# Kernel tuning notes

Measured on AMD Instinct MI355X. Metric: run time of the kernel, lower is better.

## Reference

```python
import jax, jax.numpy as jnp
import numpy as np

B_, L_, H_ = 2, 2048, 2048          # batch, seq_len, hidden_size
I_, N_, NH, P_ = 4096, 128, 64, 64   # intermediate, ssm_state, num_heads, head_dim
K_, CH = 4, 256                      # conv kernel, chunk size
DT_MIN, DT_MAX = 0.0, 1e10


def setup_inputs() -> dict:
    key = jax.random.key(0)
    ks = jax.random.split(key, 8)
    conv_dim = I_ + 2 * N_
    proj_out = 2 * (I_ + N_) + NH
    return {
        "hidden_states": jax.random.normal(ks[0], (B_, L_, H_), jnp.float32),
        "W_in": jax.random.normal(ks[1], (proj_out, H_), jnp.float32) * 0.02,
        "conv_w": jax.random.normal(ks[2], (conv_dim, 1, K_), jnp.float32) * 0.2,
        "conv_b": jnp.zeros((conv_dim,), jnp.float32),
        "dt_bias": jax.random.uniform(ks[3], (NH,), jnp.float32),
        "A_log": jnp.log(jax.random.uniform(ks[4], (NH,), jnp.float32, 1.0, 16.0)),
        "D": jnp.ones((NH,), jnp.float32),
        "norm_w": jnp.ones((I_,), jnp.float32),
        "W_out": jax.random.normal(ks[5], (H_, I_), jnp.float32) * 0.02,
    }


def _segsum(x):
    # stable segment-sum: out[..., i, j] = sum_{k=j+1..i} x[..., k] for i>=j, else -inf
    T = x.shape[-1]
    xr = jnp.broadcast_to(x[..., None], x.shape + (T,))
    lower = jnp.tril(jnp.ones((T, T), bool), -1)
    s = jnp.cumsum(jnp.where(lower, xr, 0.0), axis=-2)
    return jnp.where(jnp.tril(jnp.ones((T, T), bool)), s, -jnp.inf)


def reference(hidden_states, W_in, conv_w, conv_b, dt_bias, A_log, D, norm_w, W_out):
    b, L, _ = hidden_states.shape
    proj = hidden_states @ W_in.T                       # (b, L, 2*(I+N)+H)
    z, xBC, dt = jnp.split(proj, [I_, 2 * I_ + 2 * N_], axis=-1)

    # depthwise causal conv1d + silu
    x_t = xBC.transpose(0, 2, 1)                        # (b, conv_dim, L)
    conv = jax.lax.conv_general_dilated(
        x_t, conv_w, (1,), [(K_ - 1, 0)],
        dimension_numbers=("NCH", "OIH", "NCH"), feature_group_count=I_ + 2 * N_)
    xBC = jax.nn.silu((conv + conv_b[None, :, None]).transpose(0, 2, 1))
    x, Bm, Cm = jnp.split(xBC, [I_, I_ + N_], axis=-1)  # (b,L,I) (b,L,N) (b,L,N)

    # ---- SSD naive (chunked state-space-duality scan) ----
    A = -jnp.exp(A_log.astype(jnp.float32))             # (h,)
    dt = jnp.clip(jax.nn.softplus(dt + dt_bias), DT_MIN, DT_MAX)  # (b,L,h)
    x4 = x.reshape(b, L, NH, P_)
    pad = (-L) % CH
    padf = lambda t: jnp.pad(t, [(0, 0), (0, pad)] + [(0, 0)] * (t.ndim - 2))
    D_res = D[None, None, :, None] * padf(x4)           # (b, Lp, h, p)
    xs = padf(x4 * dt[..., None])
    Ah = padf(A[None, None, :] * dt)                    # (b, Lp, h)
    Bc, Cc = padf(Bm), padf(Cm)
    c = (L + pad) // CH
    xs = xs.reshape(b, c, CH, NH, P_)                   # (b,c,l,h,p)
    Ah = Ah.reshape(b, c, CH, NH).transpose(0, 3, 1, 2) # (b,h,c,l)
    Bc = Bc.reshape(b, c, CH, N_)
    Cc = Cc.reshape(b, c, CH, N_)

    A_cs = jnp.cumsum(Ah, axis=-1)                      # (b,h,c,l)
    Lm = jnp.exp(_segsum(Ah))                           # (b,h,c,l,l)
    # intra-chunk (diagonal block) output; B/C shared across heads (n_groups=1)
    Y_diag = jnp.einsum("bcln,bcsn,bhcls,bcshp->bclhp", Cc, Bc, Lm, xs)

    decay_states = jnp.exp(A_cs[..., -1:] - A_cs)       # (b,h,c,l)
    states = jnp.einsum("bcln,bhcl,bclhp->bchpn", Bc, decay_states, xs)
    states = jnp.concatenate([jnp.zeros_like(states[:, :1]), states], axis=1)
    decay_chunk = jnp.exp(_segsum(jnp.pad(A_cs[..., -1], [(0, 0), (0, 0), (1, 0)])))
    new_states = jnp.einsum("bhzc,bchpn->bzhpn", decay_chunk, states)
    states = new_states[:, :-1]                         # (b,c,h,p,n)
    Y_off = jnp.einsum("bcln,bchpn,bhcl->bclhp", Cc, states, jnp.exp(A_cs))

    y = (Y_diag + Y_off).reshape(b, c * CH, NH, P_) + D_res
    y = y[:, :L].reshape(b, L, I_)

    # gated RMSNorm (normalize=True: multiply by silu(residual) before norm)
    yf = y.astype(jnp.float32) * jax.nn.silu(z.astype(jnp.float32))
    yf = yf * jax.lax.rsqrt(jnp.mean(yf * yf, -1, keepdims=True) + 1e-5) * norm_w
    return yf.astype(hidden_states.dtype) @ W_out.T
```

## Files before the change

kernel.cpp:

```cpp
#include <hip/hip_runtime.h>
#include <hip/hip_bf16.h>
#include <math.h>


#define B_SZ 2
#define L_SZ 2048
#define H_SZ 2048
#define I_SZ 4096
#define N_SZ 128
#define NH_SZ 64
#define P_SZ 64
#define CH_SZ 256
#define NC_SZ 8
#define PROJ_SZ 8512
#define CONV_SZ 4352
#define XOFF 4096
#define DTOFF 8448
#define BOFF 4096
#define COFF 4224

typedef __attribute__((ext_vector_type(8))) short short8_t;
typedef __attribute__((ext_vector_type(4))) float float4_t;

#define GLDS(gp, lp)                                                   \
  __builtin_amdgcn_global_load_lds(                                    \
      (const __attribute__((address_space(1))) void*)(gp),             \
      (__attribute__((address_space(3))) void*)(lp), 16, 0, 0)

__device__ __forceinline__ float bf2f(unsigned short u) {
  union { unsigned int i; float f; } v; v.i = ((unsigned int)u) << 16; return v.f;
}
__device__ __forceinline__ unsigned short f2bf(float f) {
  union { float f; unsigned int i; } v; v.f = f;
  unsigned int b = v.i + 0x7fffu + ((v.i >> 16) & 1u);
  return (unsigned short)(b >> 16);
}
__device__ __forceinline__ void unpack8(uint4 v, float* f) {
  f[0] = bf2f((unsigned short)(v.x & 0xffffu)); f[1] = bf2f((unsigned short)(v.x >> 16));
  f[2] = bf2f((unsigned short)(v.y & 0xffffu)); f[3] = bf2f((unsigned short)(v.y >> 16));
  f[4] = bf2f((unsigned short)(v.z & 0xffffu)); f[5] = bf2f((unsigned short)(v.z >> 16));
  f[6] = bf2f((unsigned short)(v.w & 0xffffu)); f[7] = bf2f((unsigned short)(v.w >> 16));
}
__device__ __forceinline__ float silu_f(float x) { return x / (1.f + expf(-x)); }

__device__ __forceinline__ float load1(const void* p, long long e, int fp32) {
  return fp32 ? ((const float*)p)[e] : bf2f(((const unsigned short*)p)[e]);
}
__device__ __forceinline__ void load4(const void* p, long long e, int fp32, float* f) {
  if (fp32) {
    float4 a = *(const float4*)((const float*)p + e);
    f[0] = a.x; f[1] = a.y; f[2] = a.z; f[3] = a.w;
  } else {
    uint2 v = *(const uint2*)((const unsigned short*)p + e);
    f[0] = bf2f((unsigned short)(v.x & 0xffffu)); f[1] = bf2f((unsigned short)(v.x >> 16));
    f[2] = bf2f((unsigned short)(v.y & 0xffffu)); f[3] = bf2f((unsigned short)(v.y >> 16));
  }
}
__device__ __forceinline__ void load8(const void* p, long long e, int fp32, float* f) {
  if (fp32) {
    float4 a = *(const float4*)((const float*)p + e);
    float4 b = *(const float4*)((const float*)p + e + 4);
    f[0] = a.x; f[1] = a.y; f[2] = a.z; f[3] = a.w;
    f[4] = b.x; f[5] = b.y; f[6] = b.z; f[7] = b.w;
  } else {
    uint4 v = *(const uint4*)((const unsigned short*)p + e);
    unpack8(v, f);
  }
}

__global__ void detect_k(const void* p0, const void* p1, const void* p2,
                         const void* p3, const void* p4, const void* p5,
                         const void* p6, const void* p7, const void* p8,
                         int n0, int n1, int n2, int n3, int n4, int n5,
                         int n6, int n7, int n8, int* flags) {
  __shared__ int pe, po;
  const void* ps[9] = {p0, p1, p2, p3, p4, p5, p6, p7, p8};
  int ns[9] = {n0, n1, n2, n3, n4, n5, n6, n7, n8};
  int t = threadIdx.x;
  for (int i = 0; i < 9; i++) {
    if (t == 0) { pe = 0; po = 0; }
    __syncthreads();
    int S = ns[i] < 256 ? ns[i] : 256;
    if (t < S) {
      unsigned short u = ((const unsigned short*)ps[i])[t];
      int ex = (u >> 7) & 0xFF;
      int plaus = ((u & 0x7FFFu) != 0) && (ex >= 0x70) && (ex <= 0x8F);
      if (plaus) { if (t & 1) atomicAdd(&po, 1); else atomicAdd(&pe, 1); }
    }
    __syncthreads();
    if (t == 0) flags[i] = (2 * pe < po) ? 1 : 0;
    __syncthreads();
  }
  if (t == 0) { flags[14] = 0; flags[15] = 0; }
}

__global__ __launch_bounds__(256)
void cvt_bf16_k(const void* __restrict__ src, unsigned short* __restrict__ dst,
                long long n8, const int* __restrict__ flags, int fi) {
  long long g = (long long)blockIdx.x * 256 + threadIdx.x;
  if (g >= n8) return;
  long long e = g * 8;
  if (flags[fi]) {
    const float* s = (const float*)src + e;
    float4 a = *(const float4*)s;
    float4 b = *(const float4*)(s + 4);
    unsigned short o[8] = {f2bf(a.x), f2bf(a.y), f2bf(a.z), f2bf(a.w),
                           f2bf(b.x), f2bf(b.y), f2bf(b.z), f2bf(b.w)};
    *(uint4*)(dst + e) = *(const uint4*)o;
  } else {
    *(uint4*)(dst + e) = *(const uint4*)((const unsigned short*)src + e);
  }
}

#define MFMA_ACC(d, a, b) \
  d = __builtin_amdgcn_mfma_f32_16x16x32_bf16(a, b, d, 0, 0, 0)
#define LDA_FR(buf, i, kk) \
  (*(const short8_t*)&As[(buf)*16384 + (wm*128 + (i)*16 + l16)*64 + \
                         (((((kk)<<2) + quad) ^ l7) << 3)])
#define LDB_FR(buf, j, kk) \
  (*(const short8_t*)&Bs[(buf)*16384 + (wn*64 + (j)*16 + l16)*64 + \
                         (((((kk)<<2) + quad) ^ l7) << 3)])
#define STAGE_A(h, tile, buf) do {                                          \
    GLDS(aSrc[h][0] + ((long long)(tile) << 6),                             \
         &As[(buf)*16384 + (h)*8192 + (wave*16)*64]);                       \
    GLDS(aSrc[h][1] + ((long long)(tile) << 6),                             \
         &As[(buf)*16384 + (h)*8192 + (wave*16 + 8)*64]);                   \
  } while (0)
#define STAGE_B(h, tile, buf) do {                                          \
    GLDS(bSrc[h][0] + ((long long)(tile) << 6),                             \
         &Bs[(buf)*16384 + (h)*8192 + (wave*16)*64]);                       \
    GLDS(bSrc[h][1] + ((long long)(tile) << 6),                             \
         &Bs[(buf)*16384 + (h)*8192 + (wave*16 + 8)*64]);                   \
  } while (0)

__global__ __launch_bounds__(512, 2)
void gemm_8ph_k(const unsigned short* __restrict__ A,
                const unsigned short* __restrict__ B,
                unsigned short* __restrict__ C,
                int N, int K, int lda, int ldb, int ldc, int gxTiles) {
  __shared__ alignas(16) unsigned short As[2 * 256 * 64];
  __shared__ alignas(16) unsigned short Bs[2 * 256 * 64];
  const int t = threadIdx.x;
  const int lane = t & 63;
  const int wave = t >> 6;
  const int quad = lane >> 4;
  const int l16 = lane & 15;
  const int l7 = lane & 7;
  const int l3 = lane >> 3;
  const int wm = wave >> 2;
  const int wn = wave & 3;

  int id = blockIdx.x;
  const int nwg = gridDim.x;
  int swz = id;
  if ((nwg & 7) == 0) swz = (id & 7) * (nwg >> 3) + (id >> 3);
  const int band = gxTiles << 2;
  const int by = (swz & 3) + ((swz / band) << 2);
  const int bx = (swz >> 2) % gxTiles;
  const int m0 = by << 8;
  const int n0 = bx << 8;
  const int NT = K >> 6;

  const int kperm = ((l7 ^ l3) << 3);
  const unsigned short* aSrc[2][2];
  const unsigned short* bSrc[2][2];
#pragma unroll
  for (int h = 0; h < 2; ++h)
#pragma unroll
    for (int c = 0; c < 2; ++c) {
      const int rloc = h * 128 + wave * 16 + c * 8 + l3;
      aSrc[h][c] = A + (long long)(m0 + rloc) * lda + kperm;
      int bn = n0 + rloc;
      if (bn > N - 1) bn = N - 1;
      bSrc[h][c] = B + (long long)bn * ldb + kperm;
    }

  float4_t acc[8][4];
#pragma unroll
  for (int i = 0; i < 8; ++i)
#pragma unroll
    for (int j = 0; j < 4; ++j) acc[i][j] = (float4_t){0.f, 0.f, 0.f, 0.f};

  STAGE_A(0, 0, 0); STAGE_A(1, 0, 0);
  STAGE_B(0, 0, 0); STAGE_B(1, 0, 0);
  STAGE_B(0, 1, 1); STAGE_B(1, 1, 1);
  asm volatile("s_waitcnt vmcnt(4)" ::: "memory");
  __builtin_amdgcn_s_barrier();

  short8_t af[4][2], bf[4][2];
  for (int tt = 0; tt < NT; ++tt) {
    const int rb = tt & 1, nb = rb ^ 1;
#pragma unroll
    for (int i = 0; i < 4; ++i) af[i][0] = LDA_FR(rb, i, 0);
#pragma unroll
    for (int j = 0; j < 4; ++j) bf[j][0] = LDB_FR(rb, j, 0);
    if (tt + 1 < NT) STAGE_A(0, tt + 1, nb);
    asm volatile("s_waitcnt lgkmcnt(4)" ::: "memory");
    __builtin_amdgcn_s_barrier();
    asm volatile("s_waitcnt lgkmcnt(0)" ::: "memory");
    __builtin_amdgcn_s_setprio(1);
#pragma unroll
    for (int i = 0; i < 4; ++i)
#pragma unroll
      for (int j = 0; j < 4; ++j) MFMA_ACC(acc[i][j], af[i][0], bf[j][0]);
    __builtin_amdgcn_s_setprio(0);
    __builtin_amdgcn_s_barrier();
#pragma unroll
    for (int i = 0; i < 4; ++i) af[i][1] = LDA_FR(rb, i, 1);
#pragma unroll
    for (int j = 0; j < 4; ++j) bf[j][1] = LDB_FR(rb, j, 1);
    if (tt + 1 < NT) STAGE_A(1, tt + 1, nb);
    asm volatile("s_waitcnt lgkmcnt(4)" ::: "memory");
    __builtin_amdgcn_s_barrier();
    asm volatile("s_waitcnt lgkmcnt(0)" ::: "memory");
    __builtin_amdgcn_s_setprio(1);
#pragma unroll
    for (int i = 0; i < 4; ++i)
#pragma unroll
      for (int j = 0; j < 4; ++j) MFMA_ACC(acc[i][j], af[i][1], bf[j][1]);
    __builtin_amdgcn_s_setprio(0);
    __builtin_amdgcn_s_barrier();
#pragma unroll
    for (int i = 0; i < 4; ++i) af[i][0] = LDA_FR(rb, 4 + i, 0);
    if (tt + 2 < NT) STAGE_B(0, tt + 2, rb);
    __builtin_amdgcn_s_barrier();
    asm volatile("s_waitcnt lgkmcnt(0)" ::: "memory");
    __builtin_amdgcn_s_setprio(1);
#pragma unroll
    for (int i = 0; i < 4; ++i)
#pragma unroll
      for (int j = 0; j < 4; ++j) MFMA_ACC(acc[4 + i][j], af[i][0], bf[j][0]);
    __builtin_amdgcn_s_setprio(0);
    __builtin_amdgcn_s_barrier();
#pragma unroll
    for (int i = 0; i < 4; ++i) af[i][1] = LDA_FR(rb, 4 + i, 1);
    if (tt + 2 < NT) STAGE_B(1, tt + 2, rb);
    __builtin_amdgcn_s_barrier();
    asm volatile("s_waitcnt lgkmcnt(0)" ::: "memory");
    __builtin_amdgcn_s_setprio(1);
#pragma unroll
    for (int i = 0; i < 4; ++i)
#pragma unroll
      for (int j = 0; j < 4; ++j) MFMA_ACC(acc[4 + i][j], af[i][1], bf[j][1]);
    __builtin_amdgcn_s_setprio(0);
    if (tt < NT - 2) asm volatile("s_waitcnt vmcnt(4)" ::: "memory");
    else             asm volatile("s_waitcnt vmcnt(0)" ::: "memory");
    __builtin_amdgcn_s_barrier();
  }

#pragma unroll
  for (int i = 0; i < 8; ++i) {
#pragma unroll
    for (int r = 0; r < 4; ++r) {
      const int m = m0 + wm * 128 + i * 16 + quad * 4 + r;
      const long long cb = (long long)m * ldc;
#pragma unroll
      for (int j = 0; j < 4; ++j) {
        const int n = n0 + wn * 64 + j * 16 + l16;
        if (n < N) C[cb + n] = f2bf(acc[i][j][r]);
      }
    }
  }
}

#define LDA2(buf, i, kk) \
  (*(const short8_t*)&As2[(buf)*8192 + (wm*64 + (i)*16 + l16)*64 + \
                          (((((kk)<<2) + quad) ^ l7) << 3)])
#define LDB2(buf, j, kk) \
  (*(const short8_t*)&Bs2[(buf)*8192 + (wn*64 + (j)*16 + l16)*64 + \
                          (((((kk)<<2) + quad) ^ l7) << 3)])

template <int OUT_MODE>
__global__ __launch_bounds__(256, 2)
void gemm_2ph_k(const unsigned short* __restrict__ A,
                const unsigned short* __restrict__ B,
                void* __restrict__ Cptr,
                int N, int K, int lda, int ldb, int ldc, int gxTiles,
                const int* __restrict__ flags, int fo) {
  __shared__ alignas(16) unsigned short As2[2 * 128 * 64];
  __shared__ alignas(16) unsigned short Bs2[2 * 128 * 64];
  const int t = threadIdx.x;
  const int lane = t & 63;
  const int wave = t >> 6;
  const int quad = lane >> 4;
  const int l16 = lane & 15;
  const int l7 = lane & 7;
  const int l3 = lane >> 3;
  const int wm = wave >> 1;
  const int wn = wave & 1;
  const int ofp = (OUT_MODE == 2) ? flags[fo] : 0;

  int id = blockIdx.x;
  const int nwg = gridDim.x;
  int swz = id;
  if ((nwg & 7) == 0) swz = (id & 7) * (nwg >> 3) + (id >> 3);
  const int band = gxTiles << 2;
  const int by = (swz & 3) + ((swz / band) << 2);
  const int bx = (swz >> 2) % gxTiles;
  const int m0 = by << 7;
  const int n0 = bx << 7;
  const int NT = K >> 6;

  const int kperm = ((l7 ^ l3) << 3);
  const unsigned short* aSrc[4];
  const unsigned short* bSrc[4];
#pragma unroll
  for (int c = 0; c < 4; ++c) {
    aSrc[c] = A + (long long)(m0 + wave * 32 + c * 8 + l3) * lda + kperm;
    int bn = n0 + wave * 32 + c * 8 + l3;
    if (bn > N - 1) bn = N - 1;
    bSrc[c] = B + (long long)bn * ldb + kperm;
  }

  float4_t acc[4][4];
#pragma unroll
  for (int i = 0; i < 4; ++i)
#pragma unroll
    for (int j = 0; j < 4; ++j) acc[i][j] = (float4_t){0.f, 0.f, 0.f, 0.f};

#pragma unroll
  for (int c = 0; c < 4; ++c) {
    GLDS(aSrc[c], &As2[(wave * 32 + c * 8) * 64]);
    GLDS(bSrc[c], &Bs2[(wave * 32 + c * 8) * 64]);
  }
  asm volatile("s_waitcnt vmcnt(0)" ::: "memory");
  __builtin_amdgcn_s_barrier();

  short8_t af[4], bfr[4];
  for (int tt = 0; tt < NT; ++tt) {
    const int rb = tt & 1, nb = rb ^ 1;
#pragma unroll
    for (int i = 0; i < 4; ++i) af[i] = LDA2(rb, i, 0);
#pragma unroll
    for (int j = 0; j < 4; ++j) bfr[j] = LDB2(rb, j, 0);
    if (tt + 1 < NT) {
      const long long ko = (long long)(tt + 1) << 6;
#pragma unroll
      for (int c = 0; c < 4; ++c) {
        GLDS(aSrc[c] + ko, &As2[nb * 8192 + (wave * 32 + c * 8) * 64]);
        GLDS(bSrc[c] + ko, &Bs2[nb * 8192 + (wave * 32 + c * 8) * 64]);
      }
    }
    __builtin_amdgcn_s_setprio(1);
#pragma unroll
    for (int i = 0; i < 4; ++i)
#pragma unroll
      for (int j = 0; j < 4; ++j) MFMA_ACC(acc[i][j], af[i], bfr[j]);
    __builtin_amdgcn_s_setprio(0);
#pragma unroll
    for (int i = 0; i < 4; ++i) af[i] = LDA2(rb, i, 1);
#pragma unroll
    for (int j = 0; j < 4; ++j) bfr[j] = LDB2(rb, j, 1);
    __builtin_amdgcn_s_setprio(1);
#pragma unroll
    for (int i = 0; i < 4; ++i)
#pragma unroll
      for (int j = 0; j < 4; ++j) MFMA_ACC(acc[i][j], af[i], bfr[j]);
    __builtin_amdgcn_s_setprio(0);
    asm volatile("s_waitcnt vmcnt(0)" ::: "memory");
    __builtin_amdgcn_s_barrier();
  }

#pragma unroll
  for (int i = 0; i < 4; ++i) {
#pragma unroll
    for (int r = 0; r < 4; ++r) {
      const int m = m0 + wm * 64 + i * 16 + quad * 4 + r;
      const long long cb = (long long)m * ldc;
#pragma unroll
      for (int j = 0; j < 4; ++j) {
        const int n = n0 + wn * 64 + j * 16 + l16;
        if (n < N) {
          float v = acc[i][j][r];
          if (ofp) ((float*)Cptr)[cb + n] = v;
          else     ((unsigned short*)Cptr)[cb + n] = f2bf(v);
        }
      }
    }
  }
}

template <int OUT_MODE>
__global__ __launch_bounds__(256)
void gemm_bt_k(const void* __restrict__ A, const void* __restrict__ B,
               void* __restrict__ Cptr, int M, int N, int K,
               int lda, int ldb, int ldc,
               long long sA, long long sB, long long sC,
               const int* __restrict__ flags, int fa, int fb, int fo) {
  __shared__ float As[128][20];
  __shared__ float Bs[128][20];
  const int t = threadIdx.x;
  const int tx = t & 15, ty = t >> 4;
  const int m0 = blockIdx.y * 128, n0 = blockIdx.x * 128;
  const int afp = flags[fa], bfp = flags[fb];
  const int ofp = (OUT_MODE == 2) ? flags[fo] : (OUT_MODE == 1);
  const long long zoff = (long long)blockIdx.z;
  float* Cf = (float*)Cptr + zoff * sC;
  unsigned short* Cb = (unsigned short*)Cptr + zoff * sC;

  float acc[8][8];
#pragma unroll
  for (int i = 0; i < 8; i++)
#pragma unroll
    for (int j = 0; j < 8; j++) acc[i][j] = 0.f;

  const int rowS = t >> 1;
  const int kof  = (t & 1) * 8;
  const long long aRow = zoff * sA + (long long)(m0 + rowS) * lda + kof;
  const long long bRow = zoff * sB + (long long)(n0 + rowS) * ldb + kof;
  const bool bOK = (n0 + rowS) < N;

  for (int k0 = 0; k0 < K; k0 += 16) {
    float af[8], bf[8];
    load8(A, aRow + k0, afp, af);
    if (bOK) load8(B, bRow + k0, bfp, bf);
    else { bf[0]=bf[1]=bf[2]=bf[3]=bf[4]=bf[5]=bf[6]=bf[7]=0.f; }
    __syncthreads();
    *(float4*)&As[rowS][kof]     = make_float4(af[0], af[1], af[2], af[3]);
    *(float4*)&As[rowS][kof + 4] = make_float4(af[4], af[5], af[6], af[7]);
    *(float4*)&Bs[rowS][kof]     = make_float4(bf[0], bf[1], bf[2], bf[3]);
    *(float4*)&Bs[rowS][kof + 4] = make_float4(bf[4], bf[5], bf[6], bf[7]);
    __syncthreads();
#pragma unroll
    for (int kk = 0; kk < 16; kk += 2) {
      float2 a2[8], b2[8];
#pragma unroll
      for (int i = 0; i < 8; i++) a2[i] = *(const float2*)&As[ty + 16 * i][kk];
#pragma unroll
      for (int j = 0; j < 8; j++) b2[j] = *(const float2*)&Bs[tx + 16 * j][kk];
#pragma unroll
      for (int i = 0; i < 8; i++)
#pragma unroll
        for (int j = 0; j < 8; j++) {
          acc[i][j] = fmaf(a2[i].x, b2[j].x, acc[i][j]);
          acc[i][j] = fmaf(a2[i].y, b2[j].y, acc[i][j]);
        }
    }
  }
#pragma unroll
  for (int i = 0; i < 8; i++) {
    const int m = m0 + ty + 16 * i;
    const long long base = (long long)m * ldc;
#pragma unroll
    for (int j = 0; j < 8; j++) {
      const int n = n0 + tx + 16 * j;
      if (n < N) {
        if (ofp) Cf[base + n] = acc[i][j];
        else     Cb[base + n] = f2bf(acc[i][j]);
      }
    }
  }
}

__global__ __launch_bounds__(256)
void conv_silu_k(const unsigned short* __restrict__ proj,
                 const void* __restrict__ cw,
                 const void* __restrict__ cb,
                 unsigned short* __restrict__ convx,
                 const int* __restrict__ flags) {
  const int total = B_SZ * L_SZ * (CONV_SZ / 4);
  int g = blockIdx.x * 256 + threadIdx.x;
  if (g >= total) return;
  const int fw = flags[2], fb = flags[3];
  int c4 = g % (CONV_SZ / 4);
  int bl = g / (CONV_SZ / 4);
  int l = bl & (L_SZ - 1);
  int ch = c4 * 4;
  float w0[8], w1[8];
  load8(cw, (long long)ch * 4, fw, w0);
  load8(cw, (long long)ch * 4 + 8, fw, w1);
  float accv[4];
  load4(cb, ch, fb, accv);
  float acc0 = accv[0], acc1 = accv[1], acc2 = accv[2], acc3 = accv[3];
  const long long rb = (long long)(bl - l);
#pragma unroll
  for (int k = 0; k < 4; k++) {
    int ls = l - 3 + k;
    if (ls < 0) continue;
    uint2 xv = *(const uint2*)(proj + (rb + ls) * PROJ_SZ + XOFF + ch);
    float x0 = bf2f((unsigned short)(xv.x & 0xffffu));
    float x1 = bf2f((unsigned short)(xv.x >> 16));
    float x2 = bf2f((unsigned short)(xv.y & 0xffffu));
    float x3 = bf2f((unsigned short)(xv.y >> 16));
    acc0 = fmaf(x0, w0[k], acc0);
    acc1 = fmaf(x1, w0[4 + k], acc1);
    acc2 = fmaf(x2, w1[k], acc2);
    acc3 = fmaf(x3, w1[4 + k], acc3);
  }
  unsigned short o0 = f2bf(silu_f(acc0));
  unsigned short o1 = f2bf(silu_f(acc1));
  unsigned short o2 = f2bf(silu_f(acc2));
  unsigned short o3 = f2bf(silu_f(acc3));
  *(uint2*)(convx + (long long)bl * CONV_SZ + ch) =
      make_uint2((unsigned int)o0 | ((unsigned int)o1 << 16),
                 (unsigned int)o2 | ((unsigned int)o3 << 16));
}

__global__ __launch_bounds__(256)
void dt_prep_k(const unsigned short* __restrict__ proj,
               const void* __restrict__ dt_bias,
               float* __restrict__ dtv, const int* __restrict__ flags) {
  int g = blockIdx.x * 256 + threadIdx.x;
  int h = g & 63;
  long long bl = g >> 6;
  float v = bf2f(proj[bl * PROJ_SZ + DTOFF + h]) + load1(dt_bias, h, flags[4]);
  float sp = (v > 20.f) ? v : log1pf(expf(v));
  dtv[g] = sp;
}

__global__ __launch_bounds__(256)
void acs_scan_k(const float* __restrict__ dtv,
                const void* __restrict__ A_log,
                float* __restrict__ acs, const int* __restrict__ flags) {
  __shared__ float sd[256];
  int blk = blockIdx.x;
  int h = blk & 63;
  int bc = blk >> 6;
  int l = threadIdx.x;
  float Ah = -expf(load1(A_log, h, flags[5]));
  long long row = (long long)bc * CH_SZ + l;
  sd[l] = Ah * dtv[row * NH_SZ + h];
  for (int off = 1; off < 256; off <<= 1) {
    __syncthreads();
    float tv = (l >= off) ? sd[l - off] : 0.f;
    __syncthreads();
    sd[l] += tv;
  }
  acs[(long long)blk * CH_SZ + l] = sd[l];
}

__global__ __launch_bounds__(256)
void chunk_states_k(const unsigned short* __restrict__ convx,
                    const float* __restrict__ dtv,
                    const float* __restrict__ acs,
                    float* __restrict__ stc) {
  __shared__ float Bw[32][128];
  __shared__ float xw[32][64];
  int blk = blockIdx.x;
  int h = blk & 63;
  int bc = blk >> 6;
  int t = threadIdx.x;
  const int p0 = (t & 15) * 4, n0 = (t >> 4) * 8;
  const float* acsb = acs + (long long)blk * 256;
  const float alast = acsb[255];
  float acc[4][8];
#pragma unroll
  for (int i = 0; i < 4; i++)
#pragma unroll
    for (int j = 0; j < 8; j++) acc[i][j] = 0.f;
  const long long row0 = (long long)bc * 256;

  for (int lt0 = 0; lt0 < 256; lt0 += 32) {
    __syncthreads();
#pragma unroll
    for (int q = 0; q < 4; q++) {
      int idx4 = (t + 256 * q) * 4;
      int r = idx4 >> 7, n = idx4 & 127;
      uint2 v = *(const uint2*)(convx + (row0 + lt0 + r) * CONV_SZ + BOFF + n);
      Bw[r][n]     = bf2f((unsigned short)(v.x & 0xffffu));
      Bw[r][n + 1] = bf2f((unsigned short)(v.x >> 16));
      Bw[r][n + 2] = bf2f((unsigned short)(v.y & 0xffffu));
      Bw[r][n + 3] = bf2f((unsigned short)(v.y >> 16));
    }
#pragma unroll
    for (int q = 0; q < 2; q++) {
      int idx4 = (t + 256 * q) * 4;
      int r = idx4 >> 6, p = idx4 & 63;
      long long lg = row0 + lt0 + r;
      float sc = dtv[lg * NH_SZ + h] * expf(alast - acsb[lt0 + r]);
      uint2 v = *(const uint2*)(convx + lg * CONV_SZ + h * 64 + p);
      xw[r][p]     = bf2f((unsigned short)(v.x & 0xffffu)) * sc;
      xw[r][p + 1] = bf2f((unsigned short)(v.x >> 16)) * sc;
      xw[r][p + 2] = bf2f((unsigned short)(v.y & 0xffffu)) * sc;
      xw[r][p + 3] = bf2f((unsigned short)(v.y >> 16)) * sc;
    }
    __syncthreads();
#pragma unroll 4
    for (int lt = 0; lt < 32; lt++) {
      float4 xv = *(const float4*)&xw[lt][p0];
      float4 b0 = *(const float4*)&Bw[lt][n0];
      float4 b1 = *(const float4*)&Bw[lt][n0 + 4];
      float xa[4] = {xv.x, xv.y, xv.z, xv.w};
      float ba[8] = {b0.x, b0.y, b0.z, b0.w, b1.x, b1.y, b1.z, b1.w};
#pragma unroll
      for (int i = 0; i < 4; i++)
#pragma unroll
        for (int j = 0; j < 8; j++) acc[i][j] = fmaf(xa[i], ba[j], acc[i][j]);
    }
  }
  float* outb = stc + (long long)blk * 8192;
#pragma unroll
  for (int i = 0; i < 4; i++) {
    *(float4*)&outb[(p0 + i) * 128 + n0] =
        make_float4(acc[i][0], acc[i][1], acc[i][2], acc[i][3]);
    *(float4*)&outb[(p0 + i) * 128 + n0 + 4] =
        make_float4(acc[i][4], acc[i][5], acc[i][6], acc[i][7]);
  }
}

__global__ __launch_bounds__(256)
void recur_k(float* __restrict__ stc, const float* __restrict__ acs) {
  int blk = blockIdx.x;
  int b = blk >> 6, h = blk & 63;
  int t = threadIdx.x;
  float S[32];
#pragma unroll
  for (int j = 0; j < 32; j++) S[j] = 0.f;
  for (int z = 0; z < 8; z++) {
    long long bz = ((long long)b * 8 + z) * 64 + h;
    long long base = bz * 8192;
    float e = expf(acs[bz * 256 + 255]);
#pragma unroll
    for (int j = 0; j < 32; j++) {
      int idx = j * 256 + t;
      float cs = stc[base + idx];
      stc[base + idx] = S[j];
      S[j] = fmaf(e, S[j], cs);
    }
  }
}

__global__ __launch_bounds__(256)
void yod_k(const unsigned short* __restrict__ convx,
           const float* __restrict__ sti,
           const float* __restrict__ acs,
           const float* __restrict__ dtv,
           const float* __restrict__ Gmat,
           const void* __restrict__ Dw,
           float* __restrict__ y, const int* __restrict__ flags) {
  __shared__ float SIt[128][68];
  __shared__ float acs_s[256];
  __shared__ alignas(16) float ubuf[64 * 68 + 64 * 66];
  float (*xsT)[68] = (float (*)[68])ubuf;
  float (*Mt)[66]  = (float (*)[66])(ubuf + 64 * 68);
  unsigned short (*Ct)[128] = (unsigned short (*)[128])ubuf;

  int blk = blockIdx.x;
  int h = blk & 63;
  int bc = blk >> 6;
  int t = threadIdx.x;
  const int txp = t & 15, lq = t >> 4;
  const float Dh = load1(Dw, h, flags[6]);
  const float* sib = sti + (long long)blk * 8192;
#pragma unroll 4
  for (int q = 0; q < 32; q++) {
    int idx = t + 256 * q;
    SIt[idx & 127][idx >> 7] = sib[idx];
  }
  acs_s[t] = acs[(long long)blk * 256 + t];
  const long long row0 = (long long)bc * 256;
  const float* Gb = Gmat + (long long)bc * 65536;

  for (int ltile = 0; ltile < 4; ltile++) {
    __syncthreads();
#pragma unroll 4
    for (int q = 0; q < 32; q++) {
      int idx = t + 256 * q;
      int lr = idx >> 7, n = idx & 127;
      Ct[lr][n] = convx[(row0 + ltile * 64 + lr) * CONV_SZ + COFF + n];
    }
    __syncthreads();
    float accO[4][4] = {};
#pragma unroll 4
    for (int n = 0; n < 128; n++) {
      float4 sv = *(const float4*)&SIt[n][txp * 4];
      float c0 = bf2f(Ct[lq * 4 + 0][n]);
      float c1 = bf2f(Ct[lq * 4 + 1][n]);
      float c2 = bf2f(Ct[lq * 4 + 2][n]);
      float c3 = bf2f(Ct[lq * 4 + 3][n]);
      accO[0][0] = fmaf(c0, sv.x, accO[0][0]); accO[0][1] = fmaf(c0, sv.y, accO[0][1]);
      accO[0][2] = fmaf(c0, sv.z, accO[0][2]); accO[0][3] = fmaf(c0, sv.w, accO[0][3]);
      accO[1][0] = fmaf(c1, sv.x, accO[1][0]); accO[1][1] = fmaf(c1, sv.y, accO[1][1]);
      accO[1][2] = fmaf(c1, sv.z, accO[1][2]); accO[1][3] = fmaf(c1, sv.w, accO[1][3]);
      accO[2][0] = fmaf(c2, sv.x, accO[2][0]); accO[2][1] = fmaf(c2, sv.y, accO[2][1]);
      accO[2][2] = fmaf(c2, sv.z, accO[2][2]); accO[2][3] = fmaf(c2, sv.w, accO[2][3]);
      accO[3][0] = fmaf(c3, sv.x, accO[3][0]); accO[3][1] = fmaf(c3, sv.y, accO[3][1]);
      accO[3][2] = fmaf(c3, sv.z, accO[3][2]); accO[3][3] = fmaf(c3, sv.w, accO[3][3]);
    }
    float accD[4][4] = {};
    for (int stile = 0; stile <= ltile; stile++) {
      __syncthreads();
#pragma unroll 4
      for (int q = 0; q < 16; q++) {
        int idx = t + 256 * q;
        int ss = idx >> 6, p = idx & 63;
        long long row = row0 + stile * 64 + ss;
        xsT[ss][p] = bf2f(convx[row * CONV_SZ + h * 64 + p]) * dtv[row * NH_SZ + h];
      }
#pragma unroll 4
      for (int q = 0; q < 16; q++) {
        int idx = t + 256 * q;
        int lr = idx >> 6, ss = idx & 63;
        int lg = ltile * 64 + lr, sg = stile * 64 + ss;
        float m = 0.f;
        if (sg <= lg) m = Gb[(long long)lg * 256 + sg] * expf(acs_s[lg] - acs_s[sg]);
        Mt[lr][ss] = m;
      }
      __syncthreads();
#pragma unroll 4
      for (int ss = 0; ss < 64; ss++) {
        float4 xv = *(const float4*)&xsT[ss][txp * 4];
        float m0 = Mt[lq * 4 + 0][ss];
        float m1 = Mt[lq * 4 + 1][ss];
        float m2 = Mt[lq * 4 + 2][ss];
        float m3 = Mt[lq * 4 + 3][ss];
        accD[0][0] = fmaf(m0, xv.x, accD[0][0]); accD[0][1] = fmaf(m0, xv.y, accD[0][1]);
        accD[0][2] = fmaf(m0, xv.z, accD[0][2]); accD[0][3] = fmaf(m0, xv.w, accD[0][3]);
        accD[1][0] = fmaf(m1, xv.x, accD[1][0]); accD[1][1] = fmaf(m1, xv.y, accD[1][1]);
        accD[1][2] = fmaf(m1, xv.z, accD[1][2]); accD[1][3] = fmaf(m1, xv.w, accD[1][3]);
        accD[2][0] = fmaf(m2, xv.x, accD[2][0]); accD[2][1] = fmaf(m2, xv.y, accD[2][1]);
        accD[2][2] = fmaf(m2, xv.z, accD[2][2]); accD[2][3] = fmaf(m2, xv.w, accD[2][3]);
        accD[3][0] = fmaf(m3, xv.x, accD[3][0]); accD[3][1] = fmaf(m3, xv.y, accD[3][1]);
        accD[3][2] = fmaf(m3, xv.z, accD[3][2]); accD[3][3] = fmaf(m3, xv.w, accD[3][3]);
      }
    }
#pragma unroll
    for (int i = 0; i < 4; i++) {
      int lloc = ltile * 64 + lq * 4 + i;
      long long row = row0 + lloc;
      float ex = expf(acs_s[lloc]);
      uint2 xv = *(const uint2*)(convx + row * CONV_SZ + h * 64 + txp * 4);
      float4 o;
      o.x = fmaf(ex, accO[i][0], Dh * bf2f((unsigned short)(xv.x & 0xffffu))) + accD[i][0];
      o.y = fmaf(ex, accO[i][1], Dh * bf2f((unsigned short)(xv.x >> 16)))     + accD[i][1];
      o.z = fmaf(ex, accO[i][2], Dh * bf2f((unsigned short)(xv.y & 0xffffu))) + accD[i][2];
      o.w = fmaf(ex, accO[i][3], Dh * bf2f((unsigned short)(xv.y >> 16)))     + accD[i][3];
      *(float4*)&y[row * I_SZ + h * 64 + txp * 4] = o;
    }
  }
}

__global__ __launch_bounds__(256)
void norm_k(const float* __restrict__ y,
            const unsigned short* __restrict__ proj,
            const void* __restrict__ nw,
            unsigned short* __restrict__ yfb, const int* __restrict__ flags) {
  __shared__ float red[4];
  __shared__ float sc_s;
  int row = blockIdx.x;
  int t = threadIdx.x;
  const int fn = flags[7];
  const float* yr = y + (long long)row * I_SZ;
  const unsigned short* zr = proj + (long long)row * PROJ_SZ;
  float g[16];
  float ss = 0.f;
#pragma unroll
  for (int q = 0; q < 4; q++) {
    int i0 = q * 1024 + t * 4;
    float4 yv = *(const float4*)&yr[i0];
    uint2 zv = *(const uint2*)&zr[i0];
    float z0 = bf2f((unsigned short)(zv.x & 0xffffu));
    float z1 = bf2f((unsigned short)(zv.x >> 16));
    float z2 = bf2f((unsigned short)(zv.y & 0xffffu));
    float z3 = bf2f((unsigned short)(zv.y >> 16));
    float g0 = yv.x * silu_f(z0), g1 = yv.y * silu_f(z1);
    float g2 = yv.z * silu_f(z2), g3 = yv.w * silu_f(z3);
    g[q * 4 + 0] = g0; g[q * 4 + 1] = g1; g[q * 4 + 2] = g2; g[q * 4 + 3] = g3;
    ss += g0 * g0 + g1 * g1 + g2 * g2 + g3 * g3;
  }
#pragma unroll
  for (int off = 32; off > 0; off >>= 1) ss += __shfl_down(ss, off, 64);
  if ((t & 63) == 0) red[t >> 6] = ss;
  __syncthreads();
  if (t == 0) sc_s = rsqrtf((red[0] + red[1] + red[2] + red[3]) * (1.f / 4096.f) + 1e-5f);
  __syncthreads();
  float sc = sc_s;
#pragma unroll
  for (int q = 0; q < 4; q++) {
    int i0 = q * 1024 + t * 4;
    float nv[4];
    load4(nw, i0, fn, nv);
    unsigned short o0 = f2bf(g[q * 4 + 0] * sc * nv[0]);
    unsigned short o1 = f2bf(g[q * 4 + 1] * sc * nv[1]);
    unsigned short o2 = f2bf(g[q * 4 + 2] * sc * nv[2]);
    unsigned short o3 = f2bf(g[q * 4 + 3] * sc * nv[3]);
    *(uint2*)&yfb[(long long)row * I_SZ + i0] =
        make_uint2((unsigned int)o0 | ((unsigned int)o1 << 16),
                   (unsigned int)o2 | ((unsigned int)o3 << 16));
  }
}

extern "C" void kernel_launch(void* const* d_in, const int* in_sizes, int n_in,
                              void* d_out, int out_size, void* d_ws, size_t ws_size,
                              hipStream_t stream) {
  const void* hs     = d_in[0];
  const void* W_in   = d_in[1];
  const void* conv_w = d_in[2];
  const void* conv_b = d_in[3];
  const void* dt_b   = d_in[4];
  const void* A_log  = d_in[5];
  const void* Dw     = d_in[6];
  const void* nw     = d_in[7];
  const void* W_out  = d_in[8];

  char* ws = (char*)d_ws;
  size_t off = 0;
  auto alloc = [&](size_t bytes) -> void* {
    void* p = ws + off;
    off += (bytes + 255) & ~(size_t)255;
    return p;
  };
  const long long ML = (long long)B_SZ * L_SZ;
  int* flags = (int*)alloc(64);
  unsigned short* proj  = (unsigned short*)alloc(ML * PROJ_SZ * 2);
  unsigned short* convx = (unsigned short*)alloc(ML * CONV_SZ * 2);
  float* dtv  = (float*)alloc(ML * NH_SZ * 4);
  float* acsb = (float*)alloc((long long)B_SZ * NC_SZ * NH_SZ * CH_SZ * 4);
  float* Gm   = (float*)alloc((long long)B_SZ * NC_SZ * CH_SZ * CH_SZ * 4);
  float* stc  = (float*)alloc((long long)B_SZ * NC_SZ * NH_SZ * P_SZ * N_SZ * 4);
  float* yb   = (float*)alloc(ML * I_SZ * 4);
  unsigned short* yfb = (unsigned short*)stc;
  unsigned short* hs_bf   = (unsigned short*)yb;
  unsigned short* Win_bf  = (unsigned short*)yb + 8388608;
  unsigned short* Wout_bf = (unsigned short*)yb;
  (void)n_in; (void)out_size;
  if (off > ws_size) return;

  dim3 blk(256);
  detect_k<<<1, blk, 0, stream>>>(hs, W_in, conv_w, conv_b, dt_b, A_log, Dw, nw, W_out,
                                  in_sizes[0], in_sizes[1], in_sizes[2], in_sizes[3],
                                  in_sizes[4], in_sizes[5], in_sizes[6], in_sizes[7],
                                  in_sizes[8], flags);
  cvt_bf16_k<<<dim3(4096), blk, 0, stream>>>(hs, hs_bf, 1048576LL, flags, 0);
  cvt_bf16_k<<<dim3(8512), blk, 0, stream>>>(W_in, Win_bf, 2179072LL, flags, 1);
  gemm_8ph_k<<<dim3(512), dim3(512), 0, stream>>>(
      hs_bf, Win_bf, proj, PROJ_SZ, H_SZ, H_SZ, H_SZ, PROJ_SZ, 32);
  gemm_2ph_k<0><<<dim3(96), blk, 0, stream>>>(
      hs_bf, Win_bf + 8192LL * 2048, proj + 8192, 320, H_SZ,
      H_SZ, H_SZ, PROJ_SZ, 3, flags, 15);
  conv_silu_k<<<dim3((B_SZ * L_SZ * (CONV_SZ / 4) + 255) / 256), blk, 0, stream>>>(
      proj, conv_w, conv_b, convx, flags);
  dt_prep_k<<<dim3((unsigned)(ML * NH_SZ / 256)), blk, 0, stream>>>(proj, dt_b, dtv, flags);
  acs_scan_k<<<dim3(B_SZ * NC_SZ * NH_SZ), blk, 0, stream>>>(dtv, A_log, acsb, flags);
  gemm_bt_k<1><<<dim3(2, 2, 16), blk, 0, stream>>>(
      (const unsigned short*)convx + COFF, (const unsigned short*)convx + BOFF,
      Gm, 256, 256, 128, CONV_SZ, CONV_SZ, 256,
      (long long)256 * CONV_SZ, (long long)256 * CONV_SZ, 65536,
      flags, 15, 15, 15);
  chunk_states_k<<<dim3(1024), blk, 0, stream>>>(convx, dtv, acsb, stc);
  recur_k<<<dim3(B_SZ * NH_SZ), blk, 0, stream>>>(stc, acsb);
  yod_k<<<dim3(1024), blk, 0, stream>>>(convx, stc, acsb, dtv, Gm, Dw, yb, flags);
  norm_k<<<dim3((unsigned)ML), blk, 0, stream>>>(yb, proj, nw, yfb, flags);
  cvt_bf16_k<<<dim3(4096), blk, 0, stream>>>(W_out, Wout_bf, 1048576LL, flags, 8);
  gemm_2ph_k<2><<<dim3(512), blk, 0, stream>>>(
      yfb, Wout_bf, d_out, H_SZ, I_SZ, I_SZ, I_SZ, H_SZ, 16,
      flags, 0);
}
```

Before: 799.8 us.

## Split fused SSD output kernel into separate off-diagonal and diagonal kernels

The fused yod_k kernel is split into yoff_k, which writes C·states plus the D skip term, and ydiag_k, which reads y back and adds the intra-chunk masked contribution. The intent is to cut per-kernel shared memory and register pressure, which should raise occupancy for each part. In exchange the y buffer is read and written an extra time and there is one more kernel launch.

Measured after the change: 726.9 us. 1.1x faster.

```diff
diff --git a/kernel.cpp b/kernel.cpp
--- a/kernel.cpp
+++ b/kernel.cpp
@@ -621,20 +621,13 @@
 }
 
 __global__ __launch_bounds__(256)
-void yod_k(const unsigned short* __restrict__ convx,
-           const float* __restrict__ sti,
-           const float* __restrict__ acs,
-           const float* __restrict__ dtv,
-           const float* __restrict__ Gmat,
-           const void* __restrict__ Dw,
-           float* __restrict__ y, const int* __restrict__ flags) {
+void yoff_k(const unsigned short* __restrict__ convx,
+            const float* __restrict__ sti,
+            const float* __restrict__ acs,
+            const void* __restrict__ Dw,
+            float* __restrict__ y, const int* __restrict__ flags) {
   __shared__ float SIt[128][68];
-  __shared__ float acs_s[256];
-  __shared__ alignas(16) float ubuf[64 * 68 + 64 * 66];
-  float (*xsT)[68] = (float (*)[68])ubuf;
-  float (*Mt)[66]  = (float (*)[66])(ubuf + 64 * 68);
-  unsigned short (*Ct)[128] = (unsigned short (*)[128])ubuf;
-
+  __shared__ unsigned short Ct[64][128];
   int blk = blockIdx.x;
   int h = blk & 63;
   int bc = blk >> 6;
@@ -647,10 +640,8 @@
     int idx = t + 256 * q;
     SIt[idx & 127][idx >> 7] = sib[idx];
   }
-  acs_s[t] = acs[(long long)blk * 256 + t];
+  const float* acsb = acs + (long long)blk * 256;
   const long long row0 = (long long)bc * 256;
-  const float* Gb = Gmat + (long long)bc * 65536;
-
   for (int ltile = 0; ltile < 4; ltile++) {
     __syncthreads();
 #pragma unroll 4
@@ -660,7 +651,7 @@
       Ct[lr][n] = convx[(row0 + ltile * 64 + lr) * CONV_SZ + COFF + n];
     }
     __syncthreads();
-    float accO[4][4] = {};
+    float acc[4][4] = {};
 #pragma unroll 4
     for (int n = 0; n < 128; n++) {
       float4 sv = *(const float4*)&SIt[n][txp * 4];
@@ -668,16 +659,50 @@
       float c1 = bf2f(Ct[lq * 4 + 1][n]);
       float c2 = bf2f(Ct[lq * 4 + 2][n]);
       float c3 = bf2f(Ct[lq * 4 + 3][n]);
-      accO[0][0] = fmaf(c0, sv.x, accO[0][0]); accO[0][1] = fmaf(c0, sv.y, accO[0][1]);
-      accO[0][2] = fmaf(c0, sv.z, accO[0][2]); accO[0][3] = fmaf(c0, sv.w, accO[0][3]);
-      accO[1][0] = fmaf(c1, sv.x, accO[1][0]); accO[1][1] = fmaf(c1, sv.y, accO[1][1]);
-      accO[1][2] = fmaf(c1, sv.z, accO[1][2]); accO[1][3] = fmaf(c1, sv.w, accO[1][3]);
-      accO[2][0] = fmaf(c2, sv.x, accO[2][0]); accO[2][1] = fmaf(c2, sv.y, accO[2][1]);
-      accO[2][2] = fmaf(c2, sv.z, accO[2][2]); accO[2][3] = fmaf(c2, sv.w, accO[2][3]);
-      accO[3][0] = fmaf(c3, sv.x, accO[3][0]); accO[3][1] = fmaf(c3, sv.y, accO[3][1]);
-      accO[3][2] = fmaf(c3, sv.z, accO[3][2]); accO[3][3] = fmaf(c3, sv.w, accO[3][3]);
-    }
-    float accD[4][4] = {};
+      acc[0][0] = fmaf(c0, sv.x, acc[0][0]); acc[0][1] = fmaf(c0, sv.y, acc[0][1]);
+      acc[0][2] = fmaf(c0, sv.z, acc[0][2]); acc[0][3] = fmaf(c0, sv.w, acc[0][3]);
+      acc[1][0] = fmaf(c1, sv.x, acc[1][0]); acc[1][1] = fmaf(c1, sv.y, acc[1][1]);
+      acc[1][2] = fmaf(c1, sv.z, acc[1][2]); acc[1][3] = fmaf(c1, sv.w, acc[1][3]);
+      acc[2][0] = fmaf(c2, sv.x, acc[2][0]); acc[2][1] = fmaf(c2, sv.y, acc[2][1]);
+      acc[2][2] = fmaf(c2, sv.z, acc[2][2]); acc[2][3] = fmaf(c2, sv.w, acc[2][3]);
+      acc[3][0] = fmaf(c3, sv.x, acc[3][0]); acc[3][1] = fmaf(c3, sv.y, acc[3][1]);
+      acc[3][2] = fmaf(c3, sv.z, acc[3][2]); acc[3][3] = fmaf(c3, sv.w, acc[3][3]);
+    }
+#pragma unroll
+    for (int i = 0; i < 4; i++) {
+      int lloc = ltile * 64 + lq * 4 + i;
+      long long row = row0 + lloc;
+      float ex = expf(acsb[lloc]);
+      uint2 xv = *(const uint2*)(convx + row * CONV_SZ + h * 64 + txp * 4);
+      float4 o;
+      o.x = fmaf(ex, acc[i][0], Dh * bf2f((unsigned short)(xv.x & 0xffffu)));
+      o.y = fmaf(ex, acc[i][1], Dh * bf2f((unsigned short)(xv.x >> 16)));
+      o.z = fmaf(ex, acc[i][2], Dh * bf2f((unsigned short)(xv.y & 0xffffu)));
+      o.w = fmaf(ex, acc[i][3], Dh * bf2f((unsigned short)(xv.y >> 16)));
+      *(float4*)&y[row * I_SZ + h * 64 + txp * 4] = o;
+    }
+  }
+}
+
+__global__ __launch_bounds__(256)
+void ydiag_k(const unsigned short* __restrict__ convx,
+             const float* __restrict__ dtv,
+             const float* __restrict__ acs,
+             const float* __restrict__ Gmat,
+             float* __restrict__ y) {
+  __shared__ float acs_s[256];
+  __shared__ float xsT[64][68];
+  __shared__ float Mt[64][66];
+  int blk = blockIdx.x;
+  int h = blk & 63;
+  int bc = blk >> 6;
+  int t = threadIdx.x;
+  const int txp = t & 15, lq = t >> 4;
+  acs_s[t] = acs[(long long)blk * 256 + t];
+  const long long row0 = (long long)bc * 256;
+  const float* Gb = Gmat + (long long)bc * 65536;
+  for (int ltile = 0; ltile < 4; ltile++) {
+    float acc[4][4] = {};
     for (int stile = 0; stile <= ltile; stile++) {
       __syncthreads();
 #pragma unroll 4
@@ -704,28 +729,23 @@
         float m1 = Mt[lq * 4 + 1][ss];
         float m2 = Mt[lq * 4 + 2][ss];
         float m3 = Mt[lq * 4 + 3][ss];
-        accD[0][0] = fmaf(m0, xv.x, accD[0][0]); accD[0][1] = fmaf(m0, xv.y, accD[0][1]);
-        accD[0][2] = fmaf(m0, xv.z, accD[0][2]); accD[0][3] = fmaf(m0, xv.w, accD[0][3]);
-        accD[1][0] = fmaf(m1, xv.x, accD[1][0]); accD[1][1] = fmaf(m1, xv.y, accD[1][1]);
-        accD[1][2] = fmaf(m1, xv.z, accD[1][2]); accD[1][3] = fmaf(m1, xv.w, accD[1][3]);
-        accD[2][0] = fmaf(m2, xv.x, accD[2][0]); accD[2][1] = fmaf(m2, xv.y, accD[2][1]);
-        accD[2][2] = fmaf(m2, xv.z, accD[2][2]); accD[2][3] = fmaf(m2, xv.w, accD[2][3]);
-        accD[3][0] = fmaf(m3, xv.x, accD[3][0]); accD[3][1] = fmaf(m3, xv.y, accD[3][1]);
-        accD[3][2] = fmaf(m3, xv.z, accD[3][2]); accD[3][3] = fmaf(m3, xv.w, accD[3][3]);
+        acc[0][0] = fmaf(m0, xv.x, acc[0][0]); acc[0][1] = fmaf(m0, xv.y, acc[0][1]);
+        acc[0][2] = fmaf(m0, xv.z, acc[0][2]); acc[0][3] = fmaf(m0, xv.w, acc[0][3]);
+        acc[1][0] = fmaf(m1, xv.x, acc[1][0]); acc[1][1] = fmaf(m1, xv.y, acc[1][1]);
+        acc[1][2] = fmaf(m1, xv.z, acc[1][2]); acc[1][3] = fmaf(m1, xv.w, acc[1][3]);
+        acc[2][0] = fmaf(m2, xv.x, acc[2][0]); acc[2][1] = fmaf(m2, xv.y, acc[2][1]);
+        acc[2][2] = fmaf(m2, xv.z, acc[2][2]); acc[2][3] = fmaf(m2, xv.w, acc[2][3]);
+        acc[3][0] = fmaf(m3, xv.x, acc[3][0]); acc[3][1] = fmaf(m3, xv.y, acc[3][1]);
+        acc[3][2] = fmaf(m3, xv.z, acc[3][2]); acc[3][3] = fmaf(m3, xv.w, acc[3][3]);
       }
     }
 #pragma unroll
     for (int i = 0; i < 4; i++) {
-      int lloc = ltile * 64 + lq * 4 + i;
-      long long row = row0 + lloc;
-      float ex = expf(acs_s[lloc]);
-      uint2 xv = *(const uint2*)(convx + row * CONV_SZ + h * 64 + txp * 4);
-      float4 o;
-      o.x = fmaf(ex, accO[i][0], Dh * bf2f((unsigned short)(xv.x & 0xffffu))) + accD[i][0];
-      o.y = fmaf(ex, accO[i][1], Dh * bf2f((unsigned short)(xv.x >> 16)))     + accD[i][1];
-      o.z = fmaf(ex, accO[i][2], Dh * bf2f((unsigned short)(xv.y & 0xffffu))) + accD[i][2];
-      o.w = fmaf(ex, accO[i][3], Dh * bf2f((unsigned short)(xv.y >> 16)))     + accD[i][3];
-      *(float4*)&y[row * I_SZ + h * 64 + txp * 4] = o;
+      long long row = row0 + ltile * 64 + lq * 4 + i;
+      float* yp = &y[row * I_SZ + h * 64 + txp * 4];
+      float4 cur = *(float4*)yp;
+      cur.x += acc[i][0]; cur.y += acc[i][1]; cur.z += acc[i][2]; cur.w += acc[i][3];
+      *(float4*)yp = cur;
     }
   }
 }
@@ -839,7 +859,8 @@
       flags, 15, 15, 15);
   chunk_states_k<<<dim3(1024), blk, 0, stream>>>(convx, dtv, acsb, stc);
   recur_k<<<dim3(B_SZ * NH_SZ), blk, 0, stream>>>(stc, acsb);
-  yod_k<<<dim3(1024), blk, 0, stream>>>(convx, stc, acsb, dtv, Gm, Dw, yb, flags);
+  yoff_k<<<dim3(1024), blk, 0, stream>>>(convx, stc, acsb, Dw, yb, flags);
+  ydiag_k<<<dim3(1024), blk, 0, stream>>>(convx, dtv, acsb, Gm, yb);
   norm_k<<<dim3((unsigned)ML), blk, 0, stream>>>(yb, proj, nw, yfb, flags);
   cvt_bf16_k<<<dim3(4096), blk, 0, stream>>>(W_out, Wout_bf, 1048576LL, flags, 8);
   gemm_2ph_k<2><<<dim3(512), blk, 0, stream>>>(
```
